# Optimization experiments

Measured on AMD Instinct MI355X. Metric: run time of the kernel, lower is better.

Reference implementation:

```python
import jax, jax.numpy as jnp
import numpy as np

IN_F = 2048
OUT_F = 8192
NUM_BLOCKS = 2097152  # (IN_F*OUT_F)//8
K = 4096
BLOCK = 8

def setup_inputs() -> dict:
    key = jax.random.key(0)
    k1, k2, k3, k4 = jax.random.split(key, 4)
    x = jax.random.normal(k1, (4, 2048, IN_F), dtype=jnp.float32)
    codebook = jax.random.normal(k2, (K, BLOCK), dtype=jnp.float32)
    indices = jax.random.randint(k3, (NUM_BLOCKS,), 0, K, dtype=jnp.int64)
    bias = jax.random.normal(k4, (OUT_F,), dtype=jnp.float32)
    return {"x": x, "codebook": codebook, "indices": indices, "bias": bias}

def reference(x, codebook, indices, bias):
    # Dequantize: gather codewords and reassemble the full weight matrix.
    # codebook[indices]: (num_blocks, block) -> flatten -> (in_f, out_f)
    W = codebook[indices].reshape(IN_F, OUT_F)
    # GPT-2 Conv1D: out = x @ W + b  (W is (in, out), not transposed)
    out = jnp.matmul(x, W) + bias
    return out
```

## Files before the change

### kernel.cpp

```cpp
#include <hip/hip_runtime.h>
#include <hip/hip_bf16.h>

typedef unsigned short ushort_t;
typedef __attribute__((ext_vector_type(8))) short short8;
typedef __attribute__((ext_vector_type(4))) float f32x4;

#define M_DIM 8192
#define N_DIM 8192
#define K_DIM 2048
#define BM 256
#define BN 256
#define BK 64
#define NT (K_DIM / BK)

__device__ __forceinline__ ushort_t f2bf(float f) {
    union { float f; unsigned u; } v; v.f = f;
    unsigned r = v.u + 0x7fffu + ((v.u >> 16) & 1u);
    return (ushort_t)(r >> 16);
}

__device__ __forceinline__ void async_copy16(const void* g, void* l) {
    __builtin_amdgcn_global_load_lds(
        (const __attribute__((address_space(1))) void*)g,
        (__attribute__((address_space(3))) void*)l, 16, 0, 0);
}

#define BAR() __builtin_amdgcn_s_barrier()
#define LGKM0() do { asm volatile("s_waitcnt lgkmcnt(0)" ::: "memory"); \
                     __builtin_amdgcn_sched_barrier(0); } while (0)

__global__ __launch_bounds__(256) void convert_x(const float* __restrict__ x,
                                                 ushort_t* __restrict__ A) {
    int t = blockIdx.x * 256 + threadIdx.x;
    const float4* p = (const float4*)x + (size_t)t * 2;
    float4 a = p[0], b = p[1];
    short8 o;
    o[0] = (short)f2bf(a.x); o[1] = (short)f2bf(a.y);
    o[2] = (short)f2bf(a.z); o[3] = (short)f2bf(a.w);
    o[4] = (short)f2bf(b.x); o[5] = (short)f2bf(b.y);
    o[6] = (short)f2bf(b.z); o[7] = (short)f2bf(b.w);
    *(short8*)(A + (size_t)t * 8) = o;
}

__global__ __launch_bounds__(256) void dequant_wt(const int* __restrict__ indices,
                                                  const float* __restrict__ codebook,
                                                  ushort_t* __restrict__ Bt) {
    int g = blockIdx.x;
    int i = blockIdx.y * 256 + threadIdx.x;
    int idx = indices[(size_t)i * 1024 + g];
    const float4* cb = (const float4*)(codebook + (size_t)idx * 8);
    float4 lo = cb[0], hi = cb[1];
    size_t base = (size_t)g * 8 * K_DIM + i;
    Bt[base + 0 * K_DIM] = f2bf(lo.x);
    Bt[base + 1 * K_DIM] = f2bf(lo.y);
    Bt[base + 2 * K_DIM] = f2bf(lo.z);
    Bt[base + 3 * K_DIM] = f2bf(lo.w);
    Bt[base + 4 * K_DIM] = f2bf(hi.x);
    Bt[base + 5 * K_DIM] = f2bf(hi.y);
    Bt[base + 6 * K_DIM] = f2bf(hi.z);
    Bt[base + 7 * K_DIM] = f2bf(hi.w);
}

__device__ __forceinline__ void load_af4(const ushort_t* p, const int (&off)[4][2],
                                         short8 (&fr)[4][2]) {
#pragma unroll
    for (int i = 0; i < 4; ++i)
#pragma unroll
        for (int kk = 0; kk < 2; ++kk)
            fr[i][kk] = *(const short8*)((const char*)p + off[i][kk]);
}

__device__ __forceinline__ void load_bf2(const ushort_t* p, const int (&off)[2][2],
                                         short8 (&fr)[2][2]) {
#pragma unroll
    for (int j = 0; j < 2; ++j)
#pragma unroll
        for (int kk = 0; kk < 2; ++kk)
            fr[j][kk] = *(const short8*)((const char*)p + off[j][kk]);
}

__device__ __forceinline__ void mfma16(const short8 (&af)[4][2], const short8 (&bf)[2][2],
                                       f32x4 (&acc)[8][4], int I0, int J0) {
    __builtin_amdgcn_s_setprio(1);
#pragma unroll
    for (int kk = 0; kk < 2; ++kk)
#pragma unroll
        for (int i = 0; i < 4; ++i)
#pragma unroll
            for (int j = 0; j < 2; ++j)
                acc[I0 + i][J0 + j] = __builtin_amdgcn_mfma_f32_16x16x32_bf16(
                    af[i][kk], bf[j][kk], acc[I0 + i][J0 + j], 0, 0, 0);
    __builtin_amdgcn_s_setprio(0);
}

__global__ __launch_bounds__(512, 2) void gemm_256_8phase(const ushort_t* __restrict__ A,
                                                          const ushort_t* __restrict__ Bt,
                                                          const float* __restrict__ bias,
                                                          float* __restrict__ C) {
    __shared__ __align__(16) ushort_t lds_a[2][2][128 * 64];
    __shared__ __align__(16) ushort_t lds_b[2][2][128 * 64];

    const int bid = blockIdx.x;
    const int x = bid & 7;
    const int q = bid >> 3;
    const int mt = ((x >> 1) << 2) + (q & 3) + (((q >> 5) & 1) << 4);
    const int nt = ((x & 1) << 3) + ((q >> 2) & 7) + (((q >> 6) & 1) << 4);
    const int m0 = mt * BM;
    const int n0 = nt * BN;

    const int tid = threadIdx.x;
    const int lane = tid & 63;
    const int wid = tid >> 6;
    const int wm = wid >> 2, wn = wid & 3;
    const int lane15 = lane & 15, laneq = lane >> 4;

    const int G0 = tid, G1 = 512 + tid;
    const int r0 = G0 >> 3, r1 = G1 >> 3;
    const int c0 = (G0 & 7) ^ (r0 & 7), c1 = (G1 & 7) ^ (r1 & 7);
    const size_t aoff0 = (size_t)(m0 + r0) * K_DIM + c0 * 8;
    const size_t aoff1 = (size_t)(m0 + r1) * K_DIM + c1 * 8;
    const size_t boff0 = (size_t)(n0 + r0) * K_DIM + c0 * 8;
    const size_t boff1 = (size_t)(n0 + r1) * K_DIM + c1 * 8;
    const int dq0 = G0 * 16, dq1 = G1 * 16;
    const size_t HOFF = (size_t)128 * K_DIM;

#define STAGE_A(gt, hh) do { \
        char* _d = (char*)&lds_a[(gt) & 1][hh][0]; \
        async_copy16(A + aoff0 + (size_t)(hh) * HOFF + (size_t)(gt) * BK, _d + dq0); \
        async_copy16(A + aoff1 + (size_t)(hh) * HOFF + (size_t)(gt) * BK, _d + dq1); \
    } while (0)
#define STAGE_B(gt, hh) do { \
        char* _d = (char*)&lds_b[(gt) & 1][hh][0]; \
        async_copy16(Bt + boff0 + (size_t)(hh) * HOFF + (size_t)(gt) * BK, _d + dq0); \
        async_copy16(Bt + boff1 + (size_t)(hh) * HOFF + (size_t)(gt) * BK, _d + dq1); \
    } while (0)

    int offA[4][2], offB[2][2];
#pragma unroll
    for (int i = 0; i < 4; ++i) {
        int row = wm * 64 + i * 16 + lane15;
#pragma unroll
        for (int kk = 0; kk < 2; ++kk)
            offA[i][kk] = row * 128 + (((kk * 4 + laneq) ^ (row & 7)) * 16);
    }
#pragma unroll
    for (int j = 0; j < 2; ++j) {
        int row = wn * 32 + j * 16 + lane15;
#pragma unroll
        for (int kk = 0; kk < 2; ++kk)
            offB[j][kk] = row * 128 + (((kk * 4 + laneq) ^ (row & 7)) * 16);
    }

    f32x4 acc[8][4];
#pragma unroll
    for (int i = 0; i < 8; ++i)
#pragma unroll
        for (int j = 0; j < 4; ++j) acc[i][j] = (f32x4){0.f, 0.f, 0.f, 0.f};

    STAGE_A(0, 0); STAGE_A(0, 1); STAGE_B(0, 0); STAGE_B(0, 1);
    STAGE_B(1, 0); STAGE_B(1, 1);
    asm volatile("s_waitcnt vmcnt(4)" ::: "memory");
    BAR();

    short8 af[4][2], bf0[2][2], bf1[2][2];

    for (int g = 0; g < NT; ++g) {
        const int d = g & 1;
        load_af4(&lds_a[d][0][0], offA, af);
        load_bf2(&lds_b[d][0][0], offB, bf0);
        if (g + 1 < NT) { STAGE_A(g + 1, 0); STAGE_A(g + 1, 1); }
        BAR(); LGKM0();
        mfma16(af, bf0, acc, 0, 0);
        load_bf2(&lds_b[d][1][0], offB, bf1);
        BAR(); LGKM0();
        mfma16(af, bf1, acc, 0, 2);
        load_af4(&lds_a[d][1][0], offA, af);
        if (g + 2 < NT) STAGE_B(g + 2, 0);
        BAR(); LGKM0();
        mfma16(af, bf1, acc, 4, 2);
        if (g + 2 < NT) STAGE_B(g + 2, 1);
        if (g < NT - 2) { asm volatile("s_waitcnt vmcnt(4)" ::: "memory"); }
        else            { asm volatile("s_waitcnt vmcnt(0)" ::: "memory"); }
        __builtin_amdgcn_sched_barrier(0);
        BAR();
        mfma16(af, bf0, acc, 4, 0);
    }

#pragma unroll
    for (int ig = 0; ig < 8; ++ig) {
        int row = m0 + (ig >> 2) * 128 + wm * 64 + (ig & 3) * 16 + laneq * 4;
#pragma unroll
        for (int jg = 0; jg < 4; ++jg) {
            int col = n0 + (jg >> 1) * 128 + wn * 32 + (jg & 1) * 16 + lane15;
            float bv = bias[col];
            f32x4 v = acc[ig][jg];
#pragma unroll
            for (int q2 = 0; q2 < 4; ++q2)
                C[(size_t)(row + q2) * N_DIM + col] = v[q2] + bv;
        }
    }
#undef STAGE_A
#undef STAGE_B
}

extern "C" void kernel_launch(void* const* d_in, const int* in_sizes, int n_in,
                              void* d_out, int out_size, void* d_ws, size_t ws_size,
                              hipStream_t stream) {
    const float* x = (const float*)d_in[0];
    const float* codebook = (const float*)d_in[1];
    const int* indices = (const int*)d_in[2];
    const float* bias = (const float*)d_in[3];
    float* out = (float*)d_out;

    ushort_t* A  = (ushort_t*)d_ws;
    ushort_t* Bt = (ushort_t*)d_ws + (size_t)M_DIM * K_DIM;

    convert_x<<<dim3(M_DIM * K_DIM / (256 * 8)), 256, 0, stream>>>(x, A);
    dequant_wt<<<dim3(1024, 8), 256, 0, stream>>>(indices, codebook, Bt);
    gemm_256_8phase<<<dim3((M_DIM / BM) * (N_DIM / BN)), 512, 0, stream>>>(A, Bt, bias, out);
}
```

Baseline: 286.3 us.

## Prefetch next K-tile LDS fragments and relax lgkmcnt waits in GEMM loop

Restructures the 8-phase GEMM main loop so the A and B fragments for the next K tile are read from LDS during the last phase of the current iteration. Double-buffered B fragment registers are swapped by unrolling the loop by two. Partial lgkmcnt waits replace full drains so MFMAs can start while later LDS reads are still in flight. Offset computation is simplified to a base offset plus constant strides. The extra fragment registers raise VGPR pressure, which could cause spills under the 2-waves-per-SIMD launch bound.

After: 395.0 us. +38.0%, slower.

```diff
diff --git a/kernel.cpp b/kernel.cpp
--- a/kernel.cpp
+++ b/kernel.cpp
@@ -26,7 +26,7 @@
 }
 
 #define BAR() __builtin_amdgcn_s_barrier()
-#define LGKM0() do { asm volatile("s_waitcnt lgkmcnt(0)" ::: "memory"); \
+#define LGKM(n) do { asm volatile("s_waitcnt lgkmcnt(" #n ")" ::: "memory"); \
                      __builtin_amdgcn_sched_barrier(0); } while (0)
 
 __global__ __launch_bounds__(256) void convert_x(const float* __restrict__ x,
@@ -61,22 +61,22 @@
     Bt[base + 7 * K_DIM] = f2bf(hi.w);
 }
 
-__device__ __forceinline__ void load_af4(const ushort_t* p, const int (&off)[4][2],
-                                         short8 (&fr)[4][2]) {
-#pragma unroll
-    for (int i = 0; i < 4; ++i)
-#pragma unroll
-        for (int kk = 0; kk < 2; ++kk)
-            fr[i][kk] = *(const short8*)((const char*)p + off[i][kk]);
-}
-
-__device__ __forceinline__ void load_bf2(const ushort_t* p, const int (&off)[2][2],
-                                         short8 (&fr)[2][2]) {
-#pragma unroll
-    for (int j = 0; j < 2; ++j)
-#pragma unroll
-        for (int kk = 0; kk < 2; ++kk)
-            fr[j][kk] = *(const short8*)((const char*)p + off[j][kk]);
+__device__ __forceinline__ void read_a(const char* half, int o0, int o1,
+                                       short8 (&fr)[4][2]) {
+#pragma unroll
+    for (int i = 0; i < 4; ++i) {
+        fr[i][0] = *(const short8*)(half + o0 + i * 2048);
+        fr[i][1] = *(const short8*)(half + o1 + i * 2048);
+    }
+}
+
+__device__ __forceinline__ void read_b(const char* half, int o0, int o1,
+                                       short8 (&fr)[2][2]) {
+#pragma unroll
+    for (int j = 0; j < 2; ++j) {
+        fr[j][0] = *(const short8*)(half + o0 + j * 2048);
+        fr[j][1] = *(const short8*)(half + o1 + j * 2048);
+    }
 }
 
 __device__ __forceinline__ void mfma16(const short8 (&af)[4][2], const short8 (&bf)[2][2],
@@ -135,56 +135,60 @@
         async_copy16(Bt + boff1 + (size_t)(hh) * HOFF + (size_t)(gt) * BK, _d + dq1); \
     } while (0)
 
-    int offA[4][2], offB[2][2];
-#pragma unroll
-    for (int i = 0; i < 4; ++i) {
-        int row = wm * 64 + i * 16 + lane15;
-#pragma unroll
-        for (int kk = 0; kk < 2; ++kk)
-            offA[i][kk] = row * 128 + (((kk * 4 + laneq) ^ (row & 7)) * 16);
-    }
-#pragma unroll
-    for (int j = 0; j < 2; ++j) {
-        int row = wn * 32 + j * 16 + lane15;
-#pragma unroll
-        for (int kk = 0; kk < 2; ++kk)
-            offB[j][kk] = row * 128 + (((kk * 4 + laneq) ^ (row & 7)) * 16);
-    }
+    const int xa = lane15 & 7;
+    const int oa0 = (wm * 64 + lane15) * 128 + (((0 * 4 + laneq) ^ xa) * 16);
+    const int oa1 = (wm * 64 + lane15) * 128 + (((1 * 4 + laneq) ^ xa) * 16);
+    const int ob0 = (wn * 32 + lane15) * 128 + (((0 * 4 + laneq) ^ xa) * 16);
+    const int ob1 = (wn * 32 + lane15) * 128 + (((1 * 4 + laneq) ^ xa) * 16);
 
     f32x4 acc[8][4];
 #pragma unroll
     for (int i = 0; i < 8; ++i)
 #pragma unroll
         for (int j = 0; j < 4; ++j) acc[i][j] = (f32x4){0.f, 0.f, 0.f, 0.f};
+
+    short8 afX[4][2], afY[4][2], bfA[2][2], bfB[2][2], bf1[2][2];
 
     STAGE_A(0, 0); STAGE_A(0, 1); STAGE_B(0, 0); STAGE_B(0, 1);
     STAGE_B(1, 0); STAGE_B(1, 1);
     asm volatile("s_waitcnt vmcnt(4)" ::: "memory");
     BAR();
-
-    short8 af[4][2], bf0[2][2], bf1[2][2];
-
-    for (int g = 0; g < NT; ++g) {
-        const int d = g & 1;
-        load_af4(&lds_a[d][0][0], offA, af);
-        load_bf2(&lds_b[d][0][0], offB, bf0);
-        if (g + 1 < NT) { STAGE_A(g + 1, 0); STAGE_A(g + 1, 1); }
-        BAR(); LGKM0();
-        mfma16(af, bf0, acc, 0, 0);
-        load_bf2(&lds_b[d][1][0], offB, bf1);
-        BAR(); LGKM0();
-        mfma16(af, bf1, acc, 0, 2);
-        load_af4(&lds_a[d][1][0], offA, af);
-        if (g + 2 < NT) STAGE_B(g + 2, 0);
-        BAR(); LGKM0();
-        mfma16(af, bf1, acc, 4, 2);
-        if (g + 2 < NT) STAGE_B(g + 2, 1);
-        if (g < NT - 2) { asm volatile("s_waitcnt vmcnt(4)" ::: "memory"); }
-        else            { asm volatile("s_waitcnt vmcnt(0)" ::: "memory"); }
-        __builtin_amdgcn_sched_barrier(0);
-        BAR();
-        mfma16(af, bf0, acc, 4, 0);
-    }
+    read_a((const char*)&lds_a[0][0][0], oa0, oa1, afX);
+    read_b((const char*)&lds_b[0][0][0], ob0, ob1, bfA);
+
+#define KITER(g, bf0c, bf0n) do { \
+        const int d = (g) & 1; \
+         \
+        read_b((const char*)&lds_b[d][1][0], ob0, ob1, bf1); \
+        if ((g) + 1 < NT) { STAGE_A((g) + 1, 0); STAGE_A((g) + 1, 1); } \
+        BAR(); LGKM(4); \
+        mfma16(afX, bf0c, acc, 0, 0); \
+         \
+        read_a((const char*)&lds_a[d][1][0], oa0, oa1, afY); \
+        BAR(); LGKM(8); \
+        mfma16(afX, bf1, acc, 0, 2); \
+         \
+        if ((g) + 2 < NT) STAGE_B((g) + 2, 0); \
+        BAR(); LGKM(0); \
+        mfma16(afY, bf1, acc, 4, 2); \
+         \
+        if ((g) + 2 < NT) STAGE_B((g) + 2, 1); \
+        if ((g) < NT - 2) { asm volatile("s_waitcnt vmcnt(4)" ::: "memory"); } \
+        else              { asm volatile("s_waitcnt vmcnt(0)" ::: "memory"); } \
+        __builtin_amdgcn_sched_barrier(0); \
+        if ((g) + 1 < NT) { \
+            read_a((const char*)&lds_a[1 - d][0][0], oa0, oa1, afX); \
+            read_b((const char*)&lds_b[1 - d][0][0], ob0, ob1, bf0n); \
+        } \
+        BAR(); \
+        mfma16(afY, bf0c, acc, 4, 0); \
+    } while (0)
+
+    for (int g = 0; g < NT; g += 2) {
+        KITER(g, bfA, bfB);
+        KITER(g + 1, bfB, bfA);
+    }
+#undef KITER
 
 #pragma unroll
     for (int ig = 0; ig < 8; ++ig) {
```
